# Kernel optimization log

Hardware: AMD Instinct MI355X
Metric: run time of the kernel (lower is better)

The kernel has to match this reference:

```python
import jax, jax.numpy as jnp
import numpy as np

B, T, I, H, O, D = 64, 256, 256, 512, 256, 16


def setup_inputs() -> dict:
    key = jax.random.key(0)
    ks = jax.random.split(key, 7)
    bound_a = 1.0 / np.sqrt(I)
    bound_e = 1.0 / np.sqrt(H)
    xav = np.sqrt(6.0 / (H + H))  # xavier_uniform bound for lateral
    return {
        "x": jax.random.normal(ks[0], (B, T, I), dtype=jnp.float32),
        "w_afferent": jax.random.uniform(ks[1], (H, I), minval=-bound_a, maxval=bound_a, dtype=jnp.float32),
        "b_afferent": jax.random.uniform(ks[2], (H,), minval=-bound_a, maxval=bound_a, dtype=jnp.float32),
        "lateral": jax.random.uniform(ks[3], (H, H), minval=-xav, maxval=xav, dtype=jnp.float32),
        "tau": D * jax.random.uniform(ks[4], (H, H), dtype=jnp.float32) + 1.0,
        "w_efferent": jax.random.uniform(ks[5], (O, H), minval=-bound_e, maxval=bound_e, dtype=jnp.float32),
        "b_efferent": jax.random.uniform(ks[6], (O,), minval=-bound_e, maxval=bound_e, dtype=jnp.float32),
        "max_delay": D,
    }


def _forward(x, w_afferent, b_afferent, lateral, tau, w_efferent, b_efferent, max_delay):
    sigma = max_delay / 2.0
    inv_sigma = 1.0 / sigma
    batch, time, _ = x.shape
    hidden = lateral.shape[0]
    nslots = max_delay + 1

    # credit matrix: [nslots, H_out, H_in]
    tau_c = jnp.clip(tau, 1.0, float(max_delay))[None, :, :]
    d = jnp.arange(nslots, dtype=x.dtype)[:, None, None]
    credit = jax.nn.relu(-jnp.abs((d - tau_c) * inv_sigma**2) + inv_sigma)
    cm = credit * lateral[None, :, :]  # [nslots, h, i]

    slot_ids = jnp.arange(nslots)

    def step(carry, x_t):
        buf, ptr = carry  # buf: [nslots, B, H]
        h_delayed = buf[ptr]  # [B, H] (dynamic gather)
        h = jnp.tanh(x_t @ w_afferent.T + b_afferent + h_delayed)  # [B, H]
        scattered = jnp.einsum('dhi,bi->dbh', cm, h)  # [nslots, B, H]
        buf = buf + jnp.roll(scattered, ptr, axis=0)
        buf = buf * (slot_ids != ptr)[:, None, None].astype(buf.dtype)
        y_t = h_delayed @ w_efferent.T + b_efferent  # [B, O]
        return (buf, (ptr + 1) % nslots), y_t

    buf0 = jnp.zeros((nslots, batch, hidden), dtype=x.dtype)
    (_, _), ys = jax.lax.scan(step, (buf0, jnp.int32(0)), jnp.swapaxes(x, 0, 1))
    return ys[-1]  # [B, O], matches torch forward returning y[:, -1, :]


def reference(x, w_afferent, b_afferent, lateral, tau, w_efferent, b_efferent, max_delay):
    return _forward(x, w_afferent, b_afferent, lateral, tau, w_efferent, b_efferent, max_delay)
```

## Files before the change

### kernel.cpp

```cpp
#include <hip/hip_runtime.h>
#include <hip/hip_bf16.h>

typedef unsigned short u16;
typedef unsigned int u32;
typedef __bf16 bf16x8 __attribute__((ext_vector_type(8)));
typedef _Float16 f16x8 __attribute__((ext_vector_type(8)));
typedef float f32x4 __attribute__((ext_vector_type(4)));

#define B_ 64
#define T_ 256
#define I_ 256
#define H_ 512
#define O_ 256
#define D_ 16
#define NWG 128
#define CM_SCALE 64.0f
#define CM_INV   0.015625f

__device__ __forceinline__ bf16x8 ld_bf8(const u16* p){
  uint4 u = *(const uint4*)p;
  return __builtin_bit_cast(bf16x8, u);
}

__global__ __launch_bounds__(256) void k_split(const float* __restrict__ src,
    u16* __restrict__ hi, u16* __restrict__ lo, int n){
  int i = blockIdx.x*256 + threadIdx.x;
  if (i >= n) return;
  float v = src[i];
  __bf16 h = (__bf16)v;
  __bf16 l = (__bf16)(v - (float)h);
  hi[i] = __builtin_bit_cast(u16, h);
  lo[i] = __builtin_bit_cast(u16, l);
}

__global__ __launch_bounds__(256) void k_prep_cm(const float* __restrict__ tau,
    const float* __restrict__ lat, _Float16* __restrict__ cmf){
  int idx = blockIdx.x*256 + threadIdx.x;
  if (idx >= D_*H_*H_) return;
  int d = idx / (H_*H_) + 1;
  int r = idx % (H_*H_);
  float tc = fminf(fmaxf(tau[r], 1.0f), (float)D_);
  float cr = fmaxf(0.0f, 0.125f - fabsf((float)d - tc) * 0.015625f);
  cmf[idx] = (_Float16)(cr * lat[r] * CM_SCALE);
}

__global__ __launch_bounds__(256) void k_aff(const u16* __restrict__ xhi,
    const u16* __restrict__ xlo, const u16* __restrict__ wahi,
    const u16* __restrict__ walo, const float* __restrict__ ba,
    float* __restrict__ acc, float* __restrict__ aff_last){
  int g = blockIdx.x;
  int mg = g >> 2, ng = g & 3;
  int tid = threadIdx.x;
  int w = tid >> 6, l = tid & 63;
  int lr = l & 15, lk8 = (l >> 4) * 8;
  f32x4 accr[4][2];
  #pragma unroll
  for (int a=0;a<4;++a){ accr[a][0]=(f32x4){0.f,0.f,0.f,0.f}; accr[a][1]=(f32x4){0.f,0.f,0.f,0.f}; }
  #pragma unroll 1
  for (int kk = 0; kk < 8; ++kk){
    int i = kk*32 + lk8;
    bf16x8 ahi[4], alo[4];
    #pragma unroll
    for (int mt = 0; mt < 4; ++mt){
      int r = mg*64 + mt*16 + lr;
      int t = r >> 6, b = r & 63;
      size_t off = ((size_t)b*T_ + t)*I_ + i;
      ahi[mt] = ld_bf8(xhi + off);
      alo[mt] = ld_bf8(xlo + off);
    }
    #pragma unroll
    for (int nj = 0; nj < 2; ++nj){
      int ho = ng*128 + w*32 + nj*16 + lr;
      bf16x8 bhi = ld_bf8(wahi + (size_t)ho*I_ + i);
      bf16x8 blo = ld_bf8(walo + (size_t)ho*I_ + i);
      #pragma unroll
      for (int mt = 0; mt < 4; ++mt){
        accr[mt][nj] = __builtin_amdgcn_mfma_f32_16x16x32_bf16(ahi[mt], bhi, accr[mt][nj],0,0,0);
        accr[mt][nj] = __builtin_amdgcn_mfma_f32_16x16x32_bf16(alo[mt], bhi, accr[mt][nj],0,0,0);
        accr[mt][nj] = __builtin_amdgcn_mfma_f32_16x16x32_bf16(ahi[mt], blo, accr[mt][nj],0,0,0);
      }
    }
  }
  #pragma unroll
  for (int mt=0; mt<4; ++mt)
    #pragma unroll
    for (int nj=0; nj<2; ++nj){
      int ho = ng*128 + w*32 + nj*16 + lr;
      float bias = ba[ho];
      #pragma unroll
      for (int r2=0;r2<4;++r2){
        int r = mg*64 + mt*16 + (l>>4)*4 + r2;
        float v = accr[mt][nj][r2] + bias;
        acc[(size_t)r*H_ + ho] = v;
        if ((r >> 6) == T_-1) aff_last[(size_t)(r & 63)*H_ + ho] = v;
      }
    }
}

__global__ __launch_bounds__(256) void k_rec(const _Float16* __restrict__ cmf,
    float* __restrict__ acc, int* __restrict__ flags){
  __shared__ char lds[98304];
  char* ldsB = lds;
  char* ldsA = lds + 65536;
  const int g = blockIdx.x;
  const int n = g & 3;
  const int k = g >> 2;
  const int d = (k >> 1) + 1;
  const int i0 = (k & 1) * 256;
  const int tid = threadIdx.x;
  const int w = tid >> 6, l = tid & 63;
  const int lr = l & 15, lkg = l >> 4;

  for (int it = tid; it < 4096; it += 256){
    int ho = it >> 5;
    int c8 = (it & 31) * 8;
    f16x8 v = *(const f16x8*)(cmf + (((size_t)(d-1)*H_ + n*128 + ho)*H_ + i0 + c8));
    int byte = (ho*512 + c8*2) ^ ((ho & 7) << 4);
    *(f16x8*)(ldsB + byte) = v;
  }
  __syncthreads();

  const int arow  = tid >> 2;
  const int acol0 = (tid & 3) * 64;

  for (int t = 0; t < T_; ++t){
    int needed = t - d + 1;
    if (tid < 64 && needed > 0){
      while (true){
        int f0 = __hip_atomic_load(flags + 2*tid,   __ATOMIC_RELAXED, __HIP_MEMORY_SCOPE_AGENT);
        int f1 = __hip_atomic_load(flags + 2*tid+1, __ATOMIC_RELAXED, __HIP_MEMORY_SCOPE_AGENT);
        if (__all(f0 >= needed && f1 >= needed)) break;
        __builtin_amdgcn_s_sleep(1);
      }
    }
    __syncthreads();

    if (t >= d){
      {
        f32x4 arr[16];
        const float* src = acc + ((size_t)(t-d)*B_ + arow)*H_ + i0 + acol0;
        #pragma unroll
        for (int j = 0; j < 16; ++j){
          asm volatile("global_load_dwordx4 %0, %1, off sc0 sc1"
                       : "=v"(arr[j]) : "v"(src + j*4));
        }
        asm volatile("s_waitcnt vmcnt(0)" ::: "memory");
        __builtin_amdgcn_sched_barrier(0);
        #pragma unroll
        for (int c8 = 0; c8 < 8; ++c8){
          f16x8 hh;
          #pragma unroll
          for (int e = 0; e < 8; ++e){
            float x = arr[c8*2 + (e>>2)][e & 3];
            float ex = __expf(2.0f * x);
            float hv = 1.0f - __fdividef(2.0f, ex + 1.0f);
            hh[e] = (_Float16)hv;
          }
          int byte = ((arow*512) + (acol0 + c8*8)*2) ^ ((arow & 7) << 4);
          *(f16x8*)(ldsA + byte) = hh;
        }
      }
      __syncthreads();

      f32x4 accr[4][2];
      #pragma unroll
      for (int a=0;a<4;++a){ accr[a][0]=(f32x4){0.f,0.f,0.f,0.f}; accr[a][1]=(f32x4){0.f,0.f,0.f,0.f}; }
      #pragma unroll 1
      for (int kk = 0; kk < 8; ++kk){
        int kb = (kk*32 + lkg*8) * 2;
        f16x8 afr[4];
        #pragma unroll
        for (int mt = 0; mt < 4; ++mt){
          int row = mt*16 + lr;
          afr[mt] = *(const f16x8*)(ldsA + ((row*512 + kb) ^ ((row & 7) << 4)));
        }
        #pragma unroll
        for (int nj = 0; nj < 2; ++nj){
          int ho = w*32 + nj*16 + lr;
          f16x8 bfr = *(const f16x8*)(ldsB + ((ho*512 + kb) ^ ((ho & 7) << 4)));
          #pragma unroll
          for (int mt = 0; mt < 4; ++mt)
            accr[mt][nj] = __builtin_amdgcn_mfma_f32_16x16x32_f16(afr[mt], bfr, accr[mt][nj],0,0,0);
        }
      }

      float* dst = acc + (size_t)t*B_*H_ + n*128;
      #pragma unroll
      for (int mt=0; mt<4; ++mt)
        #pragma unroll
        for (int nj=0; nj<2; ++nj){
          int ho = w*32 + nj*16 + lr;
          #pragma unroll
          for (int r2=0;r2<4;++r2){
            int b = mt*16 + (l>>4)*4 + r2;
            atomicAdd(dst + (size_t)b*H_ + ho, accr[mt][nj][r2] * CM_INV);
          }
        }
    }

    asm volatile("s_waitcnt vmcnt(0)" ::: "memory");
    __syncthreads();
    if (tid == 0)
      __hip_atomic_store(flags + g, t+1, __ATOMIC_RELAXED, __HIP_MEMORY_SCOPE_AGENT);
  }
}

__global__ __launch_bounds__(256) void k_out(const float* __restrict__ acc255,
    const float* __restrict__ aff_last, const float* __restrict__ we,
    const float* __restrict__ be, float* __restrict__ y){
  int idx = blockIdx.x*256 + threadIdx.x;
  int b = idx >> 8, o = idx & 255;
  const float4* pa = (const float4*)(acc255 + (size_t)b*H_);
  const float4* pf = (const float4*)(aff_last + (size_t)b*H_);
  const float4* wb = (const float4*)(we + (size_t)o*H_);
  float s = 0.f;
  #pragma unroll 8
  for (int i2 = 0; i2 < H_/4; ++i2){
    float4 p = pa[i2], f = pf[i2], q = wb[i2];
    s += (p.x-f.x)*q.x + (p.y-f.y)*q.y + (p.z-f.z)*q.z + (p.w-f.w)*q.w;
  }
  y[idx] = s + be[o];
}

extern "C" void kernel_launch(void* const* d_in, const int* in_sizes, int n_in,
                              void* d_out, int out_size, void* d_ws, size_t ws_size,
                              hipStream_t stream){
  (void)in_sizes; (void)n_in; (void)out_size; (void)ws_size;
  const float* x   = (const float*)d_in[0];
  const float* wa  = (const float*)d_in[1];
  const float* ba  = (const float*)d_in[2];
  const float* lat = (const float*)d_in[3];
  const float* tau = (const float*)d_in[4];
  const float* we  = (const float*)d_in[5];
  const float* be  = (const float*)d_in[6];
  float* y = (float*)d_out;

  char* ws = (char*)d_ws;
  size_t cur = 0;
  auto alloc = [&](size_t sz) -> void* {
    void* p = ws + cur;
    cur += (sz + 255) & ~(size_t)255;
    return p;
  };
  int*      flags    = (int*)     alloc(4096);
  float*    acc      = (float*)   alloc((size_t)T_*B_*H_*4);
  float*    aff_last = (float*)   alloc((size_t)B_*H_*4);
  u16*      xhi      = (u16*)     alloc((size_t)B_*T_*I_*2);
  u16*      xlo      = (u16*)     alloc((size_t)B_*T_*I_*2);
  u16*      wahi     = (u16*)     alloc((size_t)H_*I_*2);
  u16*      walo     = (u16*)     alloc((size_t)H_*I_*2);
  _Float16* cmf      = (_Float16*)alloc((size_t)D_*H_*H_*2);

  hipMemsetAsync(flags, 0, 4096, stream);

  k_split<<<(B_*T_*I_+255)/256, 256, 0, stream>>>(x, xhi, xlo, B_*T_*I_);
  k_split<<<(H_*I_+255)/256,   256, 0, stream>>>(wa, wahi, walo, H_*I_);
  k_prep_cm<<<(D_*H_*H_+255)/256, 256, 0, stream>>>(tau, lat, cmf);
  k_aff<<<1024, 256, 0, stream>>>(xhi, xlo, wahi, walo, ba, acc, aff_last);
  k_rec<<<NWG, 256, 0, stream>>>(cmf, acc, flags);
  k_out<<<(B_*O_+255)/256, 256, 0, stream>>>(acc + (size_t)(T_-1)*B_*H_, aff_last, we, be, y);
}
```

Measured before the change: 3.183 ms.

## Replace per-workgroup flag polling with per-timestep counters and stagger hidden loads

Inter-workgroup synchronisation in the recurrent kernel changes. Before, 64 threads polled all 128 per-workgroup progress flags every step. Now each workgroup atomically increments a per-timestep counter, and a single thread spins on one word until it reaches the workgroup count. This is meant to cut polling traffic and wait latency on the critical serial path. The global loads of the delayed hidden state are also reordered with a per-thread rotated column offset, to spread concurrent accesses across memory channels and LDS banks.

```diff
diff --git a/kernel.cpp b/kernel.cpp
--- a/kernel.cpp
+++ b/kernel.cpp
@@ -98,7 +98,7 @@
 }
 
 __global__ __launch_bounds__(256) void k_rec(const _Float16* __restrict__ cmf,
-    float* __restrict__ acc, int* __restrict__ flags){
+    float* __restrict__ acc, int* __restrict__ ctr){
   __shared__ char lds[98304];
   char* ldsB = lds;
   char* ldsA = lds + 65536;
@@ -120,43 +120,43 @@
   }
   __syncthreads();
 
-  const int arow  = tid >> 2;
-  const int acol0 = (tid & 3) * 64;
+  const int arow = tid >> 2;
+  const int q    = tid & 3;
+  const int cofs = q + ((arow & 1) << 2);
 
   for (int t = 0; t < T_; ++t){
-    int needed = t - d + 1;
-    if (tid < 64 && needed > 0){
-      while (true){
-        int f0 = __hip_atomic_load(flags + 2*tid,   __ATOMIC_RELAXED, __HIP_MEMORY_SCOPE_AGENT);
-        int f1 = __hip_atomic_load(flags + 2*tid+1, __ATOMIC_RELAXED, __HIP_MEMORY_SCOPE_AGENT);
-        if (__all(f0 >= needed && f1 >= needed)) break;
-        __builtin_amdgcn_s_sleep(1);
-      }
-    }
-    __syncthreads();
-
     if (t >= d){
+      if (tid == 0){
+        while (__hip_atomic_load(ctr + (t-d), __ATOMIC_RELAXED, __HIP_MEMORY_SCOPE_AGENT) < NWG)
+          __builtin_amdgcn_s_sleep(1);
+      }
+      __syncthreads();
+
       {
         f32x4 arr[16];
-        const float* src = acc + ((size_t)(t-d)*B_ + arow)*H_ + i0 + acol0;
-        #pragma unroll
-        for (int j = 0; j < 16; ++j){
+        const float* srow = acc + ((size_t)(t-d)*B_ + arow)*H_ + i0;
+        #pragma unroll
+        for (int j = 0; j < 8; ++j){
+          int c = (4*j + cofs) & 31;
           asm volatile("global_load_dwordx4 %0, %1, off sc0 sc1"
-                       : "=v"(arr[j]) : "v"(src + j*4));
+                       : "=v"(arr[2*j])   : "v"(srow + c*8));
+          asm volatile("global_load_dwordx4 %0, %1, off sc0 sc1"
+                       : "=v"(arr[2*j+1]) : "v"(srow + c*8 + 4));
         }
         asm volatile("s_waitcnt vmcnt(0)" ::: "memory");
         __builtin_amdgcn_sched_barrier(0);
         #pragma unroll
-        for (int c8 = 0; c8 < 8; ++c8){
+        for (int j = 0; j < 8; ++j){
+          int c = (4*j + cofs) & 31;
           f16x8 hh;
           #pragma unroll
           for (int e = 0; e < 8; ++e){
-            float x = arr[c8*2 + (e>>2)][e & 3];
+            float x = arr[2*j + (e>>2)][e & 3];
             float ex = __expf(2.0f * x);
             float hv = 1.0f - __fdividef(2.0f, ex + 1.0f);
             hh[e] = (_Float16)hv;
           }
-          int byte = ((arow*512) + (acol0 + c8*8)*2) ^ ((arow & 7) << 4);
+          int byte = (arow*512 + c*16) ^ ((arow & 7) << 4);
           *(f16x8*)(ldsA + byte) = hh;
         }
       }
@@ -201,7 +201,7 @@
     asm volatile("s_waitcnt vmcnt(0)" ::: "memory");
     __syncthreads();
     if (tid == 0)
-      __hip_atomic_store(flags + g, t+1, __ATOMIC_RELAXED, __HIP_MEMORY_SCOPE_AGENT);
+      __hip_atomic_fetch_add(ctr + t, 1, __ATOMIC_RELAXED, __HIP_MEMORY_SCOPE_AGENT);
   }
 }
 
@@ -242,7 +242,7 @@
     cur += (sz + 255) & ~(size_t)255;
     return p;
   };
-  int*      flags    = (int*)     alloc(4096);
+  int*      ctr      = (int*)     alloc(4096);
   float*    acc      = (float*)   alloc((size_t)T_*B_*H_*4);
   float*    aff_last = (float*)   alloc((size_t)B_*H_*4);
   u16*      xhi      = (u16*)     alloc((size_t)B_*T_*I_*2);
@@ -251,12 +251,12 @@
   u16*      walo     = (u16*)     alloc((size_t)H_*I_*2);
   _Float16* cmf      = (_Float16*)alloc((size_t)D_*H_*H_*2);
 
-  hipMemsetAsync(flags, 0, 4096, stream);
+  hipMemsetAsync(ctr, 0, 4096, stream);
 
   k_split<<<(B_*T_*I_+255)/256, 256, 0, stream>>>(x, xhi, xlo, B_*T_*I_);
   k_split<<<(H_*I_+255)/256,   256, 0, stream>>>(wa, wahi, walo, H_*I_);
   k_prep_cm<<<(D_*H_*H_+255)/256, 256, 0, stream>>>(tau, lat, cmf);
   k_aff<<<1024, 256, 0, stream>>>(xhi, xlo, wahi, walo, ba, acc, aff_last);
-  k_rec<<<NWG, 256, 0, stream>>>(cmf, acc, flags);
+  k_rec<<<NWG, 256, 0, stream>>>(cmf, acc, ctr);
   k_out<<<(B_*O_+255)/256, 256, 0, stream>>>(acc + (size_t)(T_-1)*B_*H_, aff_last, we, be, y);
 }
```

Result: faster. 2.737 ms (-14.0%).
